# Performance work log

Measured on AMD Instinct MI355X. Metric: run time of the kernel, lower is better.

The kernel has to match this reference:

```python
import jax, jax.numpy as jnp
import numpy as np
import math

D_MODEL = 1024
N_HEADS = 16
D_K = D_MODEL // N_HEADS
LN_EPS = 1e-5


def _linear_params(key, d_in, d_out):
    # torch Linear stores weight as [out, in]; xavier_uniform init
    bound = math.sqrt(6.0 / (d_in + d_out))
    kw, kb = jax.random.split(key)
    W = jax.random.uniform(kw, (d_out, d_in), jnp.float32, -bound, bound)
    b = jnp.zeros((d_out,), jnp.float32)
    return W, b


def setup_inputs() -> dict:
    key = jax.random.key(0)
    ks = jax.random.split(key, 8)
    x = jax.random.normal(ks[0], (2, 2048, D_MODEL), jnp.float32)
    reasoning_state = jax.random.normal(ks[1], (2, D_MODEL), jnp.float32)
    Wq, bq = _linear_params(ks[2], D_MODEL, D_MODEL)
    Wk, bk = _linear_params(ks[3], D_MODEL, D_MODEL)
    Wv, bv = _linear_params(ks[4], D_MODEL, D_MODEL)
    Wr, br = _linear_params(ks[5], D_MODEL, D_MODEL)
    Wo, bo = _linear_params(ks[6], D_MODEL, D_MODEL)
    ln_g = jnp.ones((D_MODEL,), jnp.float32)
    ln_b = jnp.zeros((D_MODEL,), jnp.float32)
    return {"x": x, "reasoning_state": reasoning_state,
            "Wq": Wq, "bq": bq, "Wk": Wk, "bk": bk, "Wv": Wv, "bv": bv,
            "Wr": Wr, "br": br, "Wo": Wo, "bo": bo, "ln_g": ln_g, "ln_b": ln_b}


def reference(x, reasoning_state, Wq, bq, Wk, bk, Wv, bv, Wr, br, Wo, bo, ln_g, ln_b):
    B, S, D = x.shape
    H, dk = N_HEADS, D_K

    def proj(z, W, b):  # torch Linear: z @ W.T + b
        return z @ W.T + b

    # [B, H, S, dk]
    Q = proj(x, Wq, bq).reshape(B, S, H, dk).transpose(0, 2, 1, 3)
    K = proj(x, Wk, bk).reshape(B, S, H, dk).transpose(0, 2, 1, 3)
    V = proj(x, Wv, bv).reshape(B, S, H, dk).transpose(0, 2, 1, 3)

    scores = jnp.einsum('bhsd,bhtd->bhst', Q, K) / math.sqrt(dk)

    # reasoning bias: R is [B, H, 1, dk]; Q @ R^T -> [B, H, S, 1], broadcast over keys
    R = proj(reasoning_state, Wr, br).reshape(B, 1, H, dk).transpose(0, 2, 1, 3)
    scores = scores + jnp.einsum('bhsd,bhud->bhsu', Q, R)  # u == 1, broadcasts

    attn = jax.nn.softmax(scores, axis=-1)
    context = jnp.einsum('bhst,bhtd->bshd', attn, V).reshape(B, S, D)
    out = proj(context, Wo, bo)

    # residual + LayerNorm
    y = out + x
    mu = jnp.mean(y, axis=-1, keepdims=True)
    var = jnp.var(y, axis=-1, keepdims=True)
    y = (y - mu) * jax.lax.rsqrt(var + LN_EPS) * ln_g + ln_b
    return (y, attn)
```

## Files before the change

kernel.cpp:

```cpp
#include <hip/hip_runtime.h>
#include <hip/hip_bf16.h>

#define DM 1024
#define NH 16
#define DKK 64
#define SL 2048
#define NBATCH 2
#define NR (NBATCH*SL)

typedef __attribute__((ext_vector_type(8))) __bf16 bf16x8;
typedef __attribute__((ext_vector_type(4))) float f32x4;
using bf16 = __hip_bfloat16;

__global__ __launch_bounds__(256) void cvt_kernel(const float* __restrict__ src,
                                                  bf16* __restrict__ dst, int n4) {
  int stride = gridDim.x * blockDim.x;
  for (int i = blockIdx.x * blockDim.x + threadIdx.x; i < n4; i += stride) {
    float4 v = ((const float4*)src)[i];
    union { bf16 h[4]; ushort4 u; } un;
    un.h[0] = __float2bfloat16(v.x);
    un.h[1] = __float2bfloat16(v.y);
    un.h[2] = __float2bfloat16(v.z);
    un.h[3] = __float2bfloat16(v.w);
    ((ushort4*)dst)[i] = un.u;
  }
}

__global__ __launch_bounds__(256) void cvt4_kernel(
    const float* __restrict__ s0, const float* __restrict__ s1,
    const float* __restrict__ s2, const float* __restrict__ s3,
    bf16* __restrict__ d0, bf16* __restrict__ d1,
    bf16* __restrict__ d2, bf16* __restrict__ d3) {
  const int z = blockIdx.y;
  const float* src = (z == 0) ? s0 : (z == 1) ? s1 : (z == 2) ? s2 : s3;
  bf16* dst = (z == 0) ? d0 : (z == 1) ? d1 : (z == 2) ? d2 : d3;
  const int n4 = DM * DM / 4;
  int stride = gridDim.x * blockDim.x;
  for (int i = blockIdx.x * blockDim.x + threadIdx.x; i < n4; i += stride) {
    float4 v = ((const float4*)src)[i];
    union { bf16 h[4]; ushort4 u; } un;
    un.h[0] = __float2bfloat16(v.x);
    un.h[1] = __float2bfloat16(v.y);
    un.h[2] = __float2bfloat16(v.z);
    un.h[3] = __float2bfloat16(v.w);
    ((ushort4*)dst)[i] = un.u;
  }
}

__device__ __forceinline__ void gemm_core(const bf16* __restrict__ A, const bf16* __restrict__ W,
                                          int rowStart, int colStart,
                                          bf16* As, bf16* Bs, f32x4 acc[4][4]) {
  const int t = threadIdx.x;
  const int lane = t & 63, w = t >> 6;
  const int lg = lane & 15, lh = lane >> 4;
  const int wm = (w >> 1) * 64, wn = (w & 1) * 64;
#pragma unroll
  for (int i = 0; i < 4; ++i)
#pragma unroll
    for (int j = 0; j < 4; ++j) acc[i][j] = (f32x4){0.f, 0.f, 0.f, 0.f};

  for (int kt = 0; kt < DM / 32; ++kt) {
    int kb = kt * 32;
#pragma unroll
    for (int q = 0; q < 2; ++q) {
      int idx = q * 256 + t;
      int row = idx >> 2;
      int ce = (idx & 3) * 8;
      const bf16* ga = A + (size_t)(rowStart + row) * DM + kb + ce;
      const bf16* gb = W + (size_t)(colStart + row) * DM + kb + ce;
      int ldsbase = (q * 256 + w * 64) * 8;
      __builtin_amdgcn_global_load_lds((const __attribute__((address_space(1))) void*)ga,
                                       (__attribute__((address_space(3))) void*)(As + ldsbase),
                                       16, 0, 0);
      __builtin_amdgcn_global_load_lds((const __attribute__((address_space(1))) void*)gb,
                                       (__attribute__((address_space(3))) void*)(Bs + ldsbase),
                                       16, 0, 0);
    }
    __syncthreads();
    bf16x8 af[4], bfr[4];
#pragma unroll
    for (int i = 0; i < 4; ++i)
      af[i] = *(const bf16x8*)(As + (wm + i * 16 + lg) * 32 + 8 * lh);
#pragma unroll
    for (int j = 0; j < 4; ++j)
      bfr[j] = *(const bf16x8*)(Bs + (wn + j * 16 + lg) * 32 + 8 * lh);
#pragma unroll
    for (int i = 0; i < 4; ++i)
#pragma unroll
      for (int j = 0; j < 4; ++j)
        acc[i][j] = __builtin_amdgcn_mfma_f32_16x16x32_bf16(af[i], bfr[j], acc[i][j], 0, 0, 0);
    __syncthreads();
  }
}

__global__ __launch_bounds__(256) void gemm_qkv_kernel(
    const bf16* __restrict__ xb,
    const bf16* __restrict__ Wqb, const bf16* __restrict__ Wkb, const bf16* __restrict__ Wvb,
    const float* __restrict__ bq, const float* __restrict__ bk, const float* __restrict__ bv,
    bf16* __restrict__ Qb, bf16* __restrict__ Kb, bf16* __restrict__ Vt) {
  __shared__ bf16 As[128 * 32], Bs[128 * 32];
  const int z = blockIdx.z;
  const bf16* W = (z == 0) ? Wqb : (z == 1) ? Wkb : Wvb;
  const float* bias = (z == 0) ? bq : (z == 1) ? bk : bv;
  int rowStart = blockIdx.y * 128, colStart = blockIdx.x * 128;
  f32x4 acc[4][4];
  gemm_core(xb, W, rowStart, colStart, As, Bs, acc);

  const int t = threadIdx.x, lane = t & 63, w = t >> 6;
  const int lg = lane & 15, lh = lane >> 4;
  const int wm = (w >> 1) * 64, wn = (w & 1) * 64;
  if (z < 2) {
    bf16* out = (z == 0) ? Qb : Kb;
    const float sc = (z == 0) ? 0.125f : 1.0f;
#pragma unroll
    for (int i = 0; i < 4; ++i)
#pragma unroll
      for (int j = 0; j < 4; ++j) {
        int col = colStart + wn + j * 16 + lg;
        float bb = bias[col];
#pragma unroll
        for (int r = 0; r < 4; ++r) {
          int row = rowStart + wm + i * 16 + 4 * lh + r;
          out[(size_t)row * DM + col] = __float2bfloat16((acc[i][j][r] + bb) * sc);
        }
      }
  } else {
#pragma unroll
    for (int i = 0; i < 4; ++i)
#pragma unroll
      for (int j = 0; j < 4; ++j) {
        int col = colStart + wn + j * 16 + lg;
        int hh = col >> 6, d = col & 63;
        float bb = bias[col];
#pragma unroll
        for (int r = 0; r < 4; ++r) {
          int row = rowStart + wm + i * 16 + 4 * lh + r;
          int bb_i = row >> 11, s = row & 2047;
          Vt[(((size_t)(bb_i * NH + hh)) * DKK + d) * SL + s] = __float2bfloat16(acc[i][j][r] + bb);
        }
      }
  }
}

__global__ __launch_bounds__(256, 2) void attn_kernel(
    const bf16* __restrict__ Qb, const bf16* __restrict__ Kb, const bf16* __restrict__ Vt,
    float* __restrict__ attn_out, bf16* __restrict__ ctxb) {
  __shared__ bf16 Ps[128 * 128];
  __shared__ float sl[2 * 128];
  const int t = threadIdx.x, lane = t & 63, w = t >> 6;
  const int lg = lane & 15, lh = lane >> 4;

  const int L = blockIdx.x;
  const int xcd = L & 7, s_in = L >> 3;
  const int bh = xcd * 4 + (s_in >> 4);
  const int qtile = s_in & 15;
  const int b = bh >> 4, h = bh & 15;
  const int qbase = qtile * 128;
  const int wr = w >> 1, wc = w & 1;

  bf16x8 qf[4][2];
#pragma unroll
  for (int i = 0; i < 4; ++i)
#pragma unroll
    for (int ks = 0; ks < 2; ++ks)
      qf[i][ks] = *(const bf16x8*)(Qb +
          (size_t)(b * SL + qbase + wr * 64 + i * 16 + lg) * DM + h * DKK + ks * 32 + 8 * lh);

  const bf16* Kbase = Kb + (size_t)b * SL * DM + h * DKK;
  const bf16* Vtb = Vt + (size_t)bh * DKK * SL;

  float lsum[4] = {0.f, 0.f, 0.f, 0.f};
  for (int kt = 0; kt < 16; ++kt) {
    bf16x8 kf[4][2];
#pragma unroll
    for (int j = 0; j < 4; ++j)
#pragma unroll
      for (int ks = 0; ks < 2; ++ks)
        kf[j][ks] = *(const bf16x8*)(Kbase +
            (size_t)(kt * 128 + wc * 64 + j * 16 + lg) * DM + ks * 32 + 8 * lh);
    f32x4 s[4][4];
    __builtin_amdgcn_s_setprio(1);
#pragma unroll
    for (int i = 0; i < 4; ++i)
#pragma unroll
      for (int j = 0; j < 4; ++j) {
        f32x4 z = (f32x4){0.f, 0.f, 0.f, 0.f};
        z = __builtin_amdgcn_mfma_f32_16x16x32_bf16(kf[j][0], qf[i][0], z, 0, 0, 0);
        s[i][j] = __builtin_amdgcn_mfma_f32_16x16x32_bf16(kf[j][1], qf[i][1], z, 0, 0, 0);
      }
    __builtin_amdgcn_s_setprio(0);
#pragma unroll
    for (int i = 0; i < 4; ++i)
#pragma unroll
      for (int j = 0; j < 4; ++j)
#pragma unroll
        for (int r = 0; r < 4; ++r) lsum[i] += __expf(s[i][j][r]);
  }
#pragma unroll
  for (int i = 0; i < 4; ++i) {
    lsum[i] += __shfl_xor(lsum[i], 16);
    lsum[i] += __shfl_xor(lsum[i], 32);
  }
  if (lh == 0) {
#pragma unroll
    for (int i = 0; i < 4; ++i) sl[wc * 128 + wr * 64 + i * 16 + lg] = lsum[i];
  }
  __syncthreads();
  float linv[4];
#pragma unroll
  for (int i = 0; i < 4; ++i) {
    int q = wr * 64 + i * 16 + lg;
    linv[i] = 1.f / (sl[q] + sl[128 + q]);
  }
  __syncthreads();

  f32x4 cacc[4][2];
#pragma unroll
  for (int i = 0; i < 4; ++i) {
    cacc[i][0] = (f32x4){0.f, 0.f, 0.f, 0.f};
    cacc[i][1] = (f32x4){0.f, 0.f, 0.f, 0.f};
  }
  float* attn_base = attn_out + (size_t)bh * SL * SL;
  char* Pb = (char*)Ps;

  for (int kt = 0; kt < 16; ++kt) {
    bf16x8 kf[4][2];
#pragma unroll
    for (int j = 0; j < 4; ++j)
#pragma unroll
      for (int ks = 0; ks < 2; ++ks)
        kf[j][ks] = *(const bf16x8*)(Kbase +
            (size_t)(kt * 128 + wc * 64 + j * 16 + lg) * DM + ks * 32 + 8 * lh);
    f32x4 s[4][4];
    __builtin_amdgcn_s_setprio(1);
#pragma unroll
    for (int i = 0; i < 4; ++i)
#pragma unroll
      for (int j = 0; j < 4; ++j) {
        f32x4 z = (f32x4){0.f, 0.f, 0.f, 0.f};
        z = __builtin_amdgcn_mfma_f32_16x16x32_bf16(kf[j][0], qf[i][0], z, 0, 0, 0);
        s[i][j] = __builtin_amdgcn_mfma_f32_16x16x32_bf16(kf[j][1], qf[i][1], z, 0, 0, 0);
      }
    __builtin_amdgcn_s_setprio(0);
#pragma unroll
    for (int i = 0; i < 4; ++i) {
      const int q = wr * 64 + i * 16 + lg;
      const int swz = (q & 7) << 4;
#pragma unroll
      for (int j = 0; j < 4; ++j) {
        const int sk0 = wc * 64 + j * 16 + 4 * lh;
        f32x4 p4;
        p4[0] = __expf(s[i][j][0]) * linv[i];
        p4[1] = __expf(s[i][j][1]) * linv[i];
        p4[2] = __expf(s[i][j][2]) * linv[i];
        p4[3] = __expf(s[i][j][3]) * linv[i];
        __builtin_nontemporal_store(p4,
            (f32x4*)(attn_base + (size_t)(qbase + q) * SL + kt * 128 + sk0));
        union { bf16 h[4]; ushort4 u; } un;
        un.h[0] = __float2bfloat16(p4[0]);
        un.h[1] = __float2bfloat16(p4[1]);
        un.h[2] = __float2bfloat16(p4[2]);
        un.h[3] = __float2bfloat16(p4[3]);
        *(ushort4*)(Pb + ((q * 256 + sk0 * 2) ^ swz)) = un.u;
      }
    }
    __syncthreads();
    __builtin_amdgcn_s_setprio(1);
#pragma unroll
    for (int ks = 0; ks < 4; ++ks) {
      bf16x8 pf[4];
#pragma unroll
      for (int i = 0; i < 4; ++i) {
        const int q = wr * 64 + i * 16 + lg;
        pf[i] = *(const bf16x8*)(Pb + ((q * 256 + ks * 64 + lh * 16) ^ ((q & 7) << 4)));
      }
      bf16x8 vf[2];
#pragma unroll
      for (int jd = 0; jd < 2; ++jd)
        vf[jd] = *(const bf16x8*)(Vtb +
            (size_t)(wc * 32 + jd * 16 + lg) * SL + kt * 128 + ks * 32 + 8 * lh);
#pragma unroll
      for (int i = 0; i < 4; ++i)
#pragma unroll
        for (int jd = 0; jd < 2; ++jd)
          cacc[i][jd] = __builtin_amdgcn_mfma_f32_16x16x32_bf16(pf[i], vf[jd], cacc[i][jd], 0, 0, 0);
    }
    __builtin_amdgcn_s_setprio(0);
    __syncthreads();
  }

#pragma unroll
  for (int i = 0; i < 4; ++i)
#pragma unroll
    for (int jd = 0; jd < 2; ++jd)
#pragma unroll
      for (int r = 0; r < 4; ++r) {
        int row = qbase + wr * 64 + i * 16 + 4 * lh + r;
        int d = wc * 32 + jd * 16 + lg;
        ctxb[(size_t)(b * SL + row) * DM + h * DKK + d] = __float2bfloat16(cacc[i][jd][r]);
      }
}

__global__ __launch_bounds__(256) void gemm_o_kernel(
    const bf16* __restrict__ ctxb, const bf16* __restrict__ Wob, const float* __restrict__ bo,
    const float* __restrict__ xf, float* __restrict__ ypre) {
  __shared__ bf16 As[128 * 32], Bs[64 * 32];
  const int t = threadIdx.x, lane = t & 63, w = t >> 6;
  const int lg = lane & 15, lh = lane >> 4;
  const int wm = (w >> 1) * 64, wn = (w & 1) * 32;
  int rowStart = blockIdx.y * 128, colStart = blockIdx.x * 64;
  f32x4 acc[4][2];
#pragma unroll
  for (int i = 0; i < 4; ++i)
#pragma unroll
    for (int j = 0; j < 2; ++j) acc[i][j] = (f32x4){0.f, 0.f, 0.f, 0.f};

  for (int kt = 0; kt < DM / 32; ++kt) {
    int kb = kt * 32;
#pragma unroll
    for (int q = 0; q < 2; ++q) {
      int idx = q * 256 + t;
      int row = idx >> 2;
      int ce = (idx & 3) * 8;
      const bf16* ga = ctxb + (size_t)(rowStart + row) * DM + kb + ce;
      int ldsbase = (q * 256 + w * 64) * 8;
      __builtin_amdgcn_global_load_lds((const __attribute__((address_space(1))) void*)ga,
                                       (__attribute__((address_space(3))) void*)(As + ldsbase),
                                       16, 0, 0);
    }
    {
      int row = t >> 2, ce = (t & 3) * 8;
      const bf16* gb = Wob + (size_t)(colStart + row) * DM + kb + ce;
      int ldsbase = (w * 64) * 8;
      __builtin_amdgcn_global_load_lds((const __attribute__((address_space(1))) void*)gb,
                                       (__attribute__((address_space(3))) void*)(Bs + ldsbase),
                                       16, 0, 0);
    }
    __syncthreads();
    bf16x8 af[4], bfr[2];
#pragma unroll
    for (int i = 0; i < 4; ++i)
      af[i] = *(const bf16x8*)(As + (wm + i * 16 + lg) * 32 + 8 * lh);
#pragma unroll
    for (int j = 0; j < 2; ++j)
      bfr[j] = *(const bf16x8*)(Bs + (wn + j * 16 + lg) * 32 + 8 * lh);
#pragma unroll
    for (int i = 0; i < 4; ++i)
#pragma unroll
      for (int j = 0; j < 2; ++j)
        acc[i][j] = __builtin_amdgcn_mfma_f32_16x16x32_bf16(af[i], bfr[j], acc[i][j], 0, 0, 0);
    __syncthreads();
  }
#pragma unroll
  for (int i = 0; i < 4; ++i)
#pragma unroll
    for (int j = 0; j < 2; ++j) {
      int col = colStart + wn + j * 16 + lg;
      float bb = bo[col];
#pragma unroll
      for (int r = 0; r < 4; ++r) {
        int row = rowStart + wm + i * 16 + 4 * lh + r;
        ypre[(size_t)row * DM + col] = acc[i][j][r] + bb + xf[(size_t)row * DM + col];
      }
    }
}

__global__ __launch_bounds__(256) void ln_kernel(const float* __restrict__ ypre,
                                                 const float* __restrict__ g,
                                                 const float* __restrict__ bta,
                                                 float* __restrict__ out) {
  int row = blockIdx.x;
  const float* yr = ypre + (size_t)row * DM;
  int t = threadIdx.x;
  float4 v = *(const float4*)(yr + t * 4);
  float s = v.x + v.y + v.z + v.w;
  float ss = v.x * v.x + v.y * v.y + v.z * v.z + v.w * v.w;
#pragma unroll
  for (int off = 1; off < 64; off <<= 1) {
    s += __shfl_xor(s, off);
    ss += __shfl_xor(ss, off);
  }
  __shared__ float red[8];
  int w = t >> 6, lane = t & 63;
  if (lane == 0) { red[w] = s; red[4 + w] = ss; }
  __syncthreads();
  s = red[0] + red[1] + red[2] + red[3];
  ss = red[4] + red[5] + red[6] + red[7];
  float mu = s * (1.f / (float)DM);
  float var = ss * (1.f / (float)DM) - mu * mu;
  float rstd = rsqrtf(var + 1e-5f);
  float4 gv = *(const float4*)(g + t * 4);
  float4 bv = *(const float4*)(bta + t * 4);
  float4 o;
  o.x = (v.x - mu) * rstd * gv.x + bv.x;
  o.y = (v.y - mu) * rstd * gv.y + bv.y;
  o.z = (v.z - mu) * rstd * gv.z + bv.z;
  o.w = (v.w - mu) * rstd * gv.w + bv.w;
  *(float4*)(out + (size_t)row * DM + t * 4) = o;
}

extern "C" void kernel_launch(void* const* d_in, const int* in_sizes, int n_in,
                              void* d_out, int out_size, void* d_ws, size_t ws_size,
                              hipStream_t stream) {
  (void)in_sizes; (void)n_in; (void)out_size; (void)ws_size;
  const float* x = (const float*)d_in[0];
  const float* Wq = (const float*)d_in[2];
  const float* bq = (const float*)d_in[3];
  const float* Wk = (const float*)d_in[4];
  const float* bk = (const float*)d_in[5];
  const float* Wv = (const float*)d_in[6];
  const float* bv = (const float*)d_in[7];
  const float* Wo = (const float*)d_in[10];
  const float* bo = (const float*)d_in[11];
  const float* ln_g = (const float*)d_in[12];
  const float* ln_b = (const float*)d_in[13];
  float* out = (float*)d_out;

  char* ws = (char*)d_ws;
  const size_t MB = 1ull << 20;
  bf16* xb   = (bf16*)(ws + 0 * MB);
  bf16* Wqb  = (bf16*)(ws + 8 * MB);
  bf16* Wkb  = (bf16*)(ws + 10 * MB);
  bf16* Wvb  = (bf16*)(ws + 12 * MB);
  bf16* Wob  = (bf16*)(ws + 14 * MB);
  bf16* Qb   = (bf16*)(ws + 16 * MB);
  bf16* Kb   = (bf16*)(ws + 24 * MB);
  bf16* Vt   = (bf16*)(ws + 32 * MB);
  bf16* ctxb = (bf16*)(ws + 40 * MB);
  float* ypre = (float*)(ws + 48 * MB);

  float* y_out = out;
  float* attn_out = out + (size_t)NR * DM;

  cvt_kernel<<<2048, 256, 0, stream>>>(x, xb, NR * DM / 4);
  cvt4_kernel<<<dim3(256, 4), 256, 0, stream>>>(Wq, Wk, Wv, Wo, Wqb, Wkb, Wvb, Wob);

  gemm_qkv_kernel<<<dim3(8, 32, 3), 256, 0, stream>>>(xb, Wqb, Wkb, Wvb, bq, bk, bv, Qb, Kb, Vt);
  attn_kernel<<<512, 256, 0, stream>>>(Qb, Kb, Vt, attn_out, ctxb);
  gemm_o_kernel<<<dim3(16, 32), 256, 0, stream>>>(ctxb, Wob, bo, x, ypre);
  ln_kernel<<<4096, 256, 0, stream>>>(ypre, ln_g, ln_b, y_out);
}
```

Before: 308.2 us.

## Single-pass attention with full-row LDS probabilities and coalesced V transpose

Attention now computes QK once per 32-row query tile, storing unnormalized exp2 probabilities in bf16 in a 128KB LDS buffer, then normalizes and streams them to the fp32 output. The PV product is split across 8 waves by key range and reduced through LDS. V-transpose stores in the QKV GEMM are staged through swizzled LDS to give coalesced 16-byte writes, and the Q scale folds in log2(e). This removes the second QK recompute but lowers occupancy through the large LDS use, and it rounds the output probabilities through bf16.

```diff
diff --git a/kernel.cpp b/kernel.cpp
--- a/kernel.cpp
+++ b/kernel.cpp
@@ -11,6 +11,8 @@
 typedef __attribute__((ext_vector_type(8))) __bf16 bf16x8;
 typedef __attribute__((ext_vector_type(4))) float f32x4;
 using bf16 = __hip_bfloat16;
+
+#define QSCALE 0.18033688011112042f
 
 __global__ __launch_bounds__(256) void cvt_kernel(const float* __restrict__ src,
                                                   bf16* __restrict__ dst, int n4) {
@@ -98,7 +100,9 @@
     const bf16* __restrict__ Wqb, const bf16* __restrict__ Wkb, const bf16* __restrict__ Wvb,
     const float* __restrict__ bq, const float* __restrict__ bk, const float* __restrict__ bv,
     bf16* __restrict__ Qb, bf16* __restrict__ Kb, bf16* __restrict__ Vt) {
-  __shared__ bf16 As[128 * 32], Bs[128 * 32];
+  __shared__ bf16 smem[128 * 128];
+  bf16* As = smem;
+  bf16* Bs = smem + 4096;
   const int z = blockIdx.z;
   const bf16* W = (z == 0) ? Wqb : (z == 1) ? Wkb : Wvb;
   const float* bias = (z == 0) ? bq : (z == 1) ? bk : bv;
@@ -111,7 +115,7 @@
   const int wm = (w >> 1) * 64, wn = (w & 1) * 64;
   if (z < 2) {
     bf16* out = (z == 0) ? Qb : Kb;
-    const float sc = (z == 0) ? 0.125f : 1.0f;
+    const float sc = (z == 0) ? QSCALE : 1.0f;
 #pragma unroll
     for (int i = 0; i < 4; ++i)
 #pragma unroll
@@ -125,180 +129,196 @@
         }
       }
   } else {
+    char* T = (char*)smem;
 #pragma unroll
     for (int i = 0; i < 4; ++i)
 #pragma unroll
       for (int j = 0; j < 4; ++j) {
-        int col = colStart + wn + j * 16 + lg;
-        int hh = col >> 6, d = col & 63;
-        float bb = bias[col];
-#pragma unroll
-        for (int r = 0; r < 4; ++r) {
-          int row = rowStart + wm + i * 16 + 4 * lh + r;
-          int bb_i = row >> 11, s = row & 2047;
-          Vt[(((size_t)(bb_i * NH + hh)) * DKK + d) * SL + s] = __float2bfloat16(acc[i][j][r] + bb);
+        int col = wn + j * 16 + lg;
+        float bb = bias[colStart + col];
+        const int swz = (col & 7) << 4;
+#pragma unroll
+        for (int r2 = 0; r2 < 4; r2 += 2) {
+          int row = wm + i * 16 + 4 * lh + r2;
+          union { bf16 hh[2]; unsigned u; } un;
+          un.hh[0] = __float2bfloat16(acc[i][j][r2] + bb);
+          un.hh[1] = __float2bfloat16(acc[i][j][r2 + 1] + bb);
+          *(unsigned*)(T + ((col * 256 + row * 2) ^ swz)) = un.u;
         }
       }
-  }
-}
-
-__global__ __launch_bounds__(256, 2) void attn_kernel(
+    __syncthreads();
+    const int b_i = rowStart >> 11;
+    const int sbase = rowStart & 2047;
+#pragma unroll
+    for (int rd = 0; rd < 8; ++rd) {
+      int d_loc = rd * 16 + (t >> 4);
+      int s8 = (t & 15) * 8;
+      bf16x8 v = *(const bf16x8*)(T + ((d_loc * 256 + s8 * 2) ^ ((d_loc & 7) << 4)));
+      int col = colStart + d_loc;
+      int h2 = col >> 6, d = col & 63;
+      *(bf16x8*)(Vt + ((size_t)(b_i * NH + h2) * DKK + d) * SL + sbase + s8) = v;
+    }
+  }
+}
+
+__global__ __launch_bounds__(512, 2) void attn2_kernel(
     const bf16* __restrict__ Qb, const bf16* __restrict__ Kb, const bf16* __restrict__ Vt,
     float* __restrict__ attn_out, bf16* __restrict__ ctxb) {
-  __shared__ bf16 Ps[128 * 128];
-  __shared__ float sl[2 * 128];
+  __shared__ bf16 Ps[32 * 2048];
+  __shared__ float sl_s[8 * 32];
+  __shared__ float linv_s[32];
   const int t = threadIdx.x, lane = t & 63, w = t >> 6;
   const int lg = lane & 15, lh = lane >> 4;
 
   const int L = blockIdx.x;
-  const int xcd = L & 7, s_in = L >> 3;
-  const int bh = xcd * 4 + (s_in >> 4);
-  const int qtile = s_in & 15;
+  const int xcd = L & 7, idx = L >> 3;
+  const int bh = xcd * 4 + (idx >> 6);
+  const int qt = idx & 63;
   const int b = bh >> 4, h = bh & 15;
-  const int qbase = qtile * 128;
-  const int wr = w >> 1, wc = w & 1;
-
-  bf16x8 qf[4][2];
-#pragma unroll
-  for (int i = 0; i < 4; ++i)
+  const int qbase = qt * 32;
+
+  const bf16* Kbase = Kb + (size_t)b * SL * DM + h * DKK;
+  const bf16* Vtb = Vt + (size_t)bh * DKK * SL;
+  char* Pb = (char*)Ps;
+  const int kw = w * 256;
+
+  bf16x8 qf[2][2];
+#pragma unroll
+  for (int i = 0; i < 2; ++i)
 #pragma unroll
     for (int ks = 0; ks < 2; ++ks)
       qf[i][ks] = *(const bf16x8*)(Qb +
-          (size_t)(b * SL + qbase + wr * 64 + i * 16 + lg) * DM + h * DKK + ks * 32 + 8 * lh);
-
-  const bf16* Kbase = Kb + (size_t)b * SL * DM + h * DKK;
-  const bf16* Vtb = Vt + (size_t)bh * DKK * SL;
-
-  float lsum[4] = {0.f, 0.f, 0.f, 0.f};
-  for (int kt = 0; kt < 16; ++kt) {
-    bf16x8 kf[4][2];
-#pragma unroll
-    for (int j = 0; j < 4; ++j)
+          (size_t)(b * SL + qbase + i * 16 + lg) * DM + h * DKK + ks * 32 + 8 * lh);
+
+  float lsum[2] = {0.f, 0.f};
+  for (int kt = 0; kt < 8; ++kt) {
+    const int kb = kw + kt * 32;
+    bf16x8 kf[2][2];
+#pragma unroll
+    for (int jj = 0; jj < 2; ++jj)
 #pragma unroll
       for (int ks = 0; ks < 2; ++ks)
-        kf[j][ks] = *(const bf16x8*)(Kbase +
-            (size_t)(kt * 128 + wc * 64 + j * 16 + lg) * DM + ks * 32 + 8 * lh);
-    f32x4 s[4][4];
+        kf[jj][ks] = *(const bf16x8*)(Kbase +
+            (size_t)(kb + jj * 16 + lg) * DM + ks * 32 + 8 * lh);
+    f32x4 s[2][2];
     __builtin_amdgcn_s_setprio(1);
 #pragma unroll
-    for (int i = 0; i < 4; ++i)
-#pragma unroll
-      for (int j = 0; j < 4; ++j) {
+    for (int i = 0; i < 2; ++i)
+#pragma unroll
+      for (int jj = 0; jj < 2; ++jj) {
         f32x4 z = (f32x4){0.f, 0.f, 0.f, 0.f};
-        z = __builtin_amdgcn_mfma_f32_16x16x32_bf16(kf[j][0], qf[i][0], z, 0, 0, 0);
-        s[i][j] = __builtin_amdgcn_mfma_f32_16x16x32_bf16(kf[j][1], qf[i][1], z, 0, 0, 0);
+        z = __builtin_amdgcn_mfma_f32_16x16x32_bf16(kf[jj][0], qf[i][0], z, 0, 0, 0);
+        s[i][jj] = __builtin_amdgcn_mfma_f32_16x16x32_bf16(kf[jj][1], qf[i][1], z, 0, 0, 0);
       }
     __builtin_amdgcn_s_setprio(0);
 #pragma unroll
-    for (int i = 0; i < 4; ++i)
-#pragma unroll
-      for (int j = 0; j < 4; ++j)
-#pragma unroll
-        for (int r = 0; r < 4; ++r) lsum[i] += __expf(s[i][j][r]);
-  }
-#pragma unroll
-  for (int i = 0; i < 4; ++i) {
+    for (int i = 0; i < 2; ++i) {
+      const int q = i * 16 + lg;
+      const int swz = (q & 7) << 4;
+#pragma unroll
+      for (int jj = 0; jj < 2; ++jj) {
+        const int key0 = kb + jj * 16 + 4 * lh;
+        float p0 = exp2f(s[i][jj][0]);
+        float p1 = exp2f(s[i][jj][1]);
+        float p2 = exp2f(s[i][jj][2]);
+        float p3 = exp2f(s[i][jj][3]);
+        lsum[i] += (p0 + p1) + (p2 + p3);
+        union { bf16 hh[4]; ushort4 u4; } un;
+        un.hh[0] = __float2bfloat16(p0);
+        un.hh[1] = __float2bfloat16(p1);
+        un.hh[2] = __float2bfloat16(p2);
+        un.hh[3] = __float2bfloat16(p3);
+        *(ushort4*)(Pb + ((q * 4096 + key0 * 2) ^ swz)) = un.u4;
+      }
+    }
+  }
+#pragma unroll
+  for (int i = 0; i < 2; ++i) {
     lsum[i] += __shfl_xor(lsum[i], 16);
     lsum[i] += __shfl_xor(lsum[i], 32);
   }
   if (lh == 0) {
-#pragma unroll
-    for (int i = 0; i < 4; ++i) sl[wc * 128 + wr * 64 + i * 16 + lg] = lsum[i];
+    sl_s[w * 32 + lg] = lsum[0];
+    sl_s[w * 32 + 16 + lg] = lsum[1];
   }
   __syncthreads();
-  float linv[4];
-#pragma unroll
-  for (int i = 0; i < 4; ++i) {
-    int q = wr * 64 + i * 16 + lg;
-    linv[i] = 1.f / (sl[q] + sl[128 + q]);
+  if (t < 32) {
+    float tot = 0.f;
+#pragma unroll
+    for (int w8 = 0; w8 < 8; ++w8) tot += sl_s[w8 * 32 + t];
+    linv_s[t] = 1.f / tot;
   }
   __syncthreads();
 
-  f32x4 cacc[4][2];
-#pragma unroll
-  for (int i = 0; i < 4; ++i) {
-    cacc[i][0] = (f32x4){0.f, 0.f, 0.f, 0.f};
-    cacc[i][1] = (f32x4){0.f, 0.f, 0.f, 0.f};
-  }
-  float* attn_base = attn_out + (size_t)bh * SL * SL;
-  char* Pb = (char*)Ps;
-
-  for (int kt = 0; kt < 16; ++kt) {
-    bf16x8 kf[4][2];
-#pragma unroll
-    for (int j = 0; j < 4; ++j)
-#pragma unroll
-      for (int ks = 0; ks < 2; ++ks)
-        kf[j][ks] = *(const bf16x8*)(Kbase +
-            (size_t)(kt * 128 + wc * 64 + j * 16 + lg) * DM + ks * 32 + 8 * lh);
-    f32x4 s[4][4];
+  float* attn_base = attn_out + (size_t)bh * SL * SL + (size_t)qbase * SL;
+#pragma unroll
+  for (int rd = 0; rd < 16; ++rd) {
+    int id2 = rd * 512 + t;
+    int q = id2 >> 8;
+    int kcol = (id2 & 255) * 8;
+    union { bf16x8 v; ushort us[8]; } pu;
+    pu.v = *(const bf16x8*)(Pb + ((q * 4096 + kcol * 2) ^ ((q & 7) << 4)));
+    float li = linv_s[q];
+    f32x4 lo, hi;
+#pragma unroll
+    for (int e = 0; e < 4; ++e) {
+      lo[e] = __uint_as_float((unsigned)pu.us[e] << 16) * li;
+      hi[e] = __uint_as_float((unsigned)pu.us[e + 4] << 16) * li;
+    }
+    f32x4* dst = (f32x4*)(attn_base + (size_t)q * SL + kcol);
+    __builtin_nontemporal_store(lo, dst);
+    __builtin_nontemporal_store(hi, dst + 1);
+  }
+
+  f32x4 acc[2][4];
+#pragma unroll
+  for (int i = 0; i < 2; ++i)
+#pragma unroll
+    for (int jd = 0; jd < 4; ++jd) acc[i][jd] = (f32x4){0.f, 0.f, 0.f, 0.f};
+  for (int ks8 = 0; ks8 < 8; ++ks8) {
+    const int kb = kw + ks8 * 32;
+    bf16x8 pf[2];
+#pragma unroll
+    for (int i = 0; i < 2; ++i) {
+      const int q = i * 16 + lg;
+      pf[i] = *(const bf16x8*)(Pb + ((q * 4096 + (kb + 8 * lh) * 2) ^ ((q & 7) << 4)));
+    }
+    bf16x8 vf[4];
+#pragma unroll
+    for (int jd = 0; jd < 4; ++jd)
+      vf[jd] = *(const bf16x8*)(Vtb + (size_t)(jd * 16 + lg) * SL + kb + 8 * lh);
     __builtin_amdgcn_s_setprio(1);
 #pragma unroll
-    for (int i = 0; i < 4; ++i)
-#pragma unroll
-      for (int j = 0; j < 4; ++j) {
-        f32x4 z = (f32x4){0.f, 0.f, 0.f, 0.f};
-        z = __builtin_amdgcn_mfma_f32_16x16x32_bf16(kf[j][0], qf[i][0], z, 0, 0, 0);
-        s[i][j] = __builtin_amdgcn_mfma_f32_16x16x32_bf16(kf[j][1], qf[i][1], z, 0, 0, 0);
-      }
+    for (int i = 0; i < 2; ++i)
+#pragma unroll
+      for (int jd = 0; jd < 4; ++jd)
+        acc[i][jd] = __builtin_amdgcn_mfma_f32_16x16x32_bf16(pf[i], vf[jd], acc[i][jd], 0, 0, 0);
     __builtin_amdgcn_s_setprio(0);
-#pragma unroll
-    for (int i = 0; i < 4; ++i) {
-      const int q = wr * 64 + i * 16 + lg;
-      const int swz = (q & 7) << 4;
-#pragma unroll
-      for (int j = 0; j < 4; ++j) {
-        const int sk0 = wc * 64 + j * 16 + 4 * lh;
-        f32x4 p4;
-        p4[0] = __expf(s[i][j][0]) * linv[i];
-        p4[1] = __expf(s[i][j][1]) * linv[i];
-        p4[2] = __expf(s[i][j][2]) * linv[i];
-        p4[3] = __expf(s[i][j][3]) * linv[i];
-        __builtin_nontemporal_store(p4,
-            (f32x4*)(attn_base + (size_t)(qbase + q) * SL + kt * 128 + sk0));
-        union { bf16 h[4]; ushort4 u; } un;
-        un.h[0] = __float2bfloat16(p4[0]);
-        un.h[1] = __float2bfloat16(p4[1]);
-        un.h[2] = __float2bfloat16(p4[2]);
-        un.h[3] = __float2bfloat16(p4[3]);
-        *(ushort4*)(Pb + ((q * 256 + sk0 * 2) ^ swz)) = un.u;
-      }
-    }
-    __syncthreads();
-    __builtin_amdgcn_s_setprio(1);
-#pragma unroll
-    for (int ks = 0; ks < 4; ++ks) {
-      bf16x8 pf[4];
-#pragma unroll
-      for (int i = 0; i < 4; ++i) {
-        const int q = wr * 64 + i * 16 + lg;
-        pf[i] = *(const bf16x8*)(Pb + ((q * 256 + ks * 64 + lh * 16) ^ ((q & 7) << 4)));
-      }
-      bf16x8 vf[2];
-#pragma unroll
-      for (int jd = 0; jd < 2; ++jd)
-        vf[jd] = *(const bf16x8*)(Vtb +
-            (size_t)(wc * 32 + jd * 16 + lg) * SL + kt * 128 + ks * 32 + 8 * lh);
-#pragma unroll
-      for (int i = 0; i < 4; ++i)
-#pragma unroll
-        for (int jd = 0; jd < 2; ++jd)
-          cacc[i][jd] = __builtin_amdgcn_mfma_f32_16x16x32_bf16(pf[i], vf[jd], cacc[i][jd], 0, 0, 0);
-    }
-    __builtin_amdgcn_s_setprio(0);
-    __syncthreads();
-  }
-
-#pragma unroll
-  for (int i = 0; i < 4; ++i)
-#pragma unroll
-    for (int jd = 0; jd < 2; ++jd)
-#pragma unroll
-      for (int r = 0; r < 4; ++r) {
-        int row = qbase + wr * 64 + i * 16 + 4 * lh + r;
-        int d = wc * 32 + jd * 16 + lg;
-        ctxb[(size_t)(b * SL + row) * DM + h * DKK + d] = __float2bfloat16(cacc[i][jd][r]);
-      }
+  }
+  __syncthreads();
+
+  float* part = (float*)Ps;
+#pragma unroll
+  for (int i = 0; i < 2; ++i)
+#pragma unroll
+    for (int jd = 0; jd < 4; ++jd)
+#pragma unroll
+      for (int r = 0; r < 4; ++r)
+        part[w * 2048 + (i * 16 + 4 * lh + r) * 64 + jd * 16 + lg] = acc[i][jd][r];
+  __syncthreads();
+
+  {
+    int e = t * 4;
+    int q = e >> 6, d0 = e & 63;
+    f32x4 sum = (f32x4){0.f, 0.f, 0.f, 0.f};
+#pragma unroll
+    for (int w8 = 0; w8 < 8; ++w8) sum += *(const f32x4*)(part + w8 * 2048 + e);
+    float li = linv_s[q];
+    union { bf16 hh[4]; ushort4 u4; } un;
+#pragma unroll
+    for (int r = 0; r < 4; ++r) un.hh[r] = __float2bfloat16(sum[r] * li);
+    *(ushort4*)(ctxb + (size_t)(b * SL + qbase + q) * DM + h * DKK + d0) = un.u4;
+  }
 }
 
 __global__ __launch_bounds__(256) void gemm_o_kernel(
@@ -436,7 +456,7 @@
   cvt4_kernel<<<dim3(256, 4), 256, 0, stream>>>(Wq, Wk, Wv, Wo, Wqb, Wkb, Wvb, Wob);
 
   gemm_qkv_kernel<<<dim3(8, 32, 3), 256, 0, stream>>>(xb, Wqb, Wkb, Wvb, bq, bk, bv, Qb, Kb, Vt);
-  attn_kernel<<<512, 256, 0, stream>>>(Qb, Kb, Vt, attn_out, ctxb);
+  attn2_kernel<<<2048, 512, 0, stream>>>(Qb, Kb, Vt, attn_out, ctxb);
   gemm_o_kernel<<<dim3(16, 32), 256, 0, stream>>>(ctxb, Wob, bo, x, ypre);
   ln_kernel<<<4096, 256, 0, stream>>>(ypre, ln_g, ln_b, y_out);
 }
```

Result: slower. 316.7 us (+2.8%).

## Split attention into denominator and write kernels, stage V transpose through LDS

Applied to the files above, without the earlier changes.

Splits the two-pass attention into one kernel that computes softmax denominators and one that writes probabilities and context. The split frees the write kernel's registers and LDS from the reduction state. The V-transpose epilogue now stages through swizzled shared memory so global stores are coalesced 16-byte writes along the sequence. Q is pre-scaled by log2(e)/8 so exp2f can replace __expf, and the per-tile barriers become explicit lgkmcnt waits plus s_barrier, dropping the trailing sync. Risks include an extra launch, an extra global round trip for the denominators, and a possible race on the P buffer now that the end-of-loop barrier is gone.

```diff
diff --git a/kernel.cpp b/kernel.cpp
--- a/kernel.cpp
+++ b/kernel.cpp
@@ -11,6 +11,14 @@
 typedef __attribute__((ext_vector_type(8))) __bf16 bf16x8;
 typedef __attribute__((ext_vector_type(4))) float f32x4;
 using bf16 = __hip_bfloat16;
+
+#define QSCALE 0.18033688011112042f
+
+#define LGKM_BARRIER() do { \
+  asm volatile("s_waitcnt lgkmcnt(0)" ::: "memory"); \
+  __builtin_amdgcn_s_barrier(); \
+  __builtin_amdgcn_sched_barrier(0); \
+} while (0)
 
 __global__ __launch_bounds__(256) void cvt_kernel(const float* __restrict__ src,
                                                   bf16* __restrict__ dst, int n4) {
@@ -98,7 +106,9 @@
     const bf16* __restrict__ Wqb, const bf16* __restrict__ Wkb, const bf16* __restrict__ Wvb,
     const float* __restrict__ bq, const float* __restrict__ bk, const float* __restrict__ bv,
     bf16* __restrict__ Qb, bf16* __restrict__ Kb, bf16* __restrict__ Vt) {
-  __shared__ bf16 As[128 * 32], Bs[128 * 32];
+  __shared__ bf16 smem[128 * 128];
+  bf16* As = smem;
+  bf16* Bs = smem + 4096;
   const int z = blockIdx.z;
   const bf16* W = (z == 0) ? Wqb : (z == 1) ? Wkb : Wvb;
   const float* bias = (z == 0) ? bq : (z == 1) ? bk : bv;
@@ -111,7 +121,7 @@
   const int wm = (w >> 1) * 64, wn = (w & 1) * 64;
   if (z < 2) {
     bf16* out = (z == 0) ? Qb : Kb;
-    const float sc = (z == 0) ? 0.125f : 1.0f;
+    const float sc = (z == 0) ? QSCALE : 1.0f;
 #pragma unroll
     for (int i = 0; i < 4; ++i)
 #pragma unroll
@@ -125,31 +135,45 @@
         }
       }
   } else {
+    char* T = (char*)smem;
+    __syncthreads();
 #pragma unroll
     for (int i = 0; i < 4; ++i)
 #pragma unroll
       for (int j = 0; j < 4; ++j) {
-        int col = colStart + wn + j * 16 + lg;
-        int hh = col >> 6, d = col & 63;
-        float bb = bias[col];
-#pragma unroll
-        for (int r = 0; r < 4; ++r) {
-          int row = rowStart + wm + i * 16 + 4 * lh + r;
-          int bb_i = row >> 11, s = row & 2047;
-          Vt[(((size_t)(bb_i * NH + hh)) * DKK + d) * SL + s] = __float2bfloat16(acc[i][j][r] + bb);
+        int col = wn + j * 16 + lg;
+        float bb = bias[colStart + col];
+        const int swz = (col & 7) << 4;
+#pragma unroll
+        for (int r2 = 0; r2 < 4; r2 += 2) {
+          int row = wm + i * 16 + 4 * lh + r2;
+          union { bf16 hh[2]; unsigned u; } un;
+          un.hh[0] = __float2bfloat16(acc[i][j][r2] + bb);
+          un.hh[1] = __float2bfloat16(acc[i][j][r2 + 1] + bb);
+          *(unsigned*)(T + ((col * 256 + row * 2) ^ swz)) = un.u;
         }
       }
-  }
-}
-
-__global__ __launch_bounds__(256, 2) void attn_kernel(
-    const bf16* __restrict__ Qb, const bf16* __restrict__ Kb, const bf16* __restrict__ Vt,
-    float* __restrict__ attn_out, bf16* __restrict__ ctxb) {
-  __shared__ bf16 Ps[128 * 128];
+    __syncthreads();
+    const int b_i = rowStart >> 11;
+    const int sbase = rowStart & 2047;
+#pragma unroll
+    for (int rd = 0; rd < 8; ++rd) {
+      int d_loc = rd * 16 + (t >> 4);
+      int s8 = (t & 15) * 8;
+      bf16x8 v = *(const bf16x8*)(T + ((d_loc * 256 + s8 * 2) ^ ((d_loc & 7) << 4)));
+      int col = colStart + d_loc;
+      int h2 = col >> 6, d = col & 63;
+      *(bf16x8*)(Vt + ((size_t)(b_i * NH + h2) * DKK + d) * SL + sbase + s8) = v;
+    }
+  }
+}
+
+__global__ __launch_bounds__(256, 2) void attn_den_kernel(
+    const bf16* __restrict__ Qb, const bf16* __restrict__ Kb,
+    float* __restrict__ linv_g) {
   __shared__ float sl[2 * 128];
   const int t = threadIdx.x, lane = t & 63, w = t >> 6;
   const int lg = lane & 15, lh = lane >> 4;
-
   const int L = blockIdx.x;
   const int xcd = L & 7, s_in = L >> 3;
   const int bh = xcd * 4 + (s_in >> 4);
@@ -167,7 +191,6 @@
           (size_t)(b * SL + qbase + wr * 64 + i * 16 + lg) * DM + h * DKK + ks * 32 + 8 * lh);
 
   const bf16* Kbase = Kb + (size_t)b * SL * DM + h * DKK;
-  const bf16* Vtb = Vt + (size_t)bh * DKK * SL;
 
   float lsum[4] = {0.f, 0.f, 0.f, 0.f};
   for (int kt = 0; kt < 16; ++kt) {
@@ -194,7 +217,7 @@
 #pragma unroll
       for (int j = 0; j < 4; ++j)
 #pragma unroll
-        for (int r = 0; r < 4; ++r) lsum[i] += __expf(s[i][j][r]);
+        for (int r = 0; r < 4; ++r) lsum[i] += exp2f(s[i][j][r]);
   }
 #pragma unroll
   for (int i = 0; i < 4; ++i) {
@@ -206,13 +229,43 @@
     for (int i = 0; i < 4; ++i) sl[wc * 128 + wr * 64 + i * 16 + lg] = lsum[i];
   }
   __syncthreads();
+  if (t < 128) {
+    linv_g[(size_t)bh * SL + qbase + t] = 1.f / (sl[t] + sl[128 + t]);
+  }
+}
+
+__global__ __launch_bounds__(256, 2) void attn_wr_kernel(
+    const bf16* __restrict__ Qb, const bf16* __restrict__ Kb, const bf16* __restrict__ Vt,
+    const float* __restrict__ linv_g,
+    float* __restrict__ attn_out, bf16* __restrict__ ctxb) {
+  __shared__ bf16 Ps[128 * 128];
+  const int t = threadIdx.x, lane = t & 63, w = t >> 6;
+  const int lg = lane & 15, lh = lane >> 4;
+  const int L = blockIdx.x;
+  const int xcd = L & 7, s_in = L >> 3;
+  const int bh = xcd * 4 + (s_in >> 4);
+  const int qtile = s_in & 15;
+  const int b = bh >> 4, h = bh & 15;
+  const int qbase = qtile * 128;
+  const int wr = w >> 1, wc = w & 1;
+
+  bf16x8 qf[4][2];
+#pragma unroll
+  for (int i = 0; i < 4; ++i)
+#pragma unroll
+    for (int ks = 0; ks < 2; ++ks)
+      qf[i][ks] = *(const bf16x8*)(Qb +
+          (size_t)(b * SL + qbase + wr * 64 + i * 16 + lg) * DM + h * DKK + ks * 32 + 8 * lh);
+
   float linv[4];
 #pragma unroll
-  for (int i = 0; i < 4; ++i) {
-    int q = wr * 64 + i * 16 + lg;
-    linv[i] = 1.f / (sl[q] + sl[128 + q]);
-  }
-  __syncthreads();
+  for (int i = 0; i < 4; ++i)
+    linv[i] = linv_g[(size_t)bh * SL + qbase + wr * 64 + i * 16 + lg];
+
+  const bf16* Kbase = Kb + (size_t)b * SL * DM + h * DKK;
+  const bf16* Vtb = Vt + (size_t)bh * DKK * SL;
+  float* attn_base = attn_out + (size_t)bh * SL * SL;
+  char* Pb = (char*)Ps;
 
   f32x4 cacc[4][2];
 #pragma unroll
@@ -220,8 +273,6 @@
     cacc[i][0] = (f32x4){0.f, 0.f, 0.f, 0.f};
     cacc[i][1] = (f32x4){0.f, 0.f, 0.f, 0.f};
   }
-  float* attn_base = attn_out + (size_t)bh * SL * SL;
-  char* Pb = (char*)Ps;
 
   for (int kt = 0; kt < 16; ++kt) {
     bf16x8 kf[4][2];
@@ -242,6 +293,9 @@
         s[i][j] = __builtin_amdgcn_mfma_f32_16x16x32_bf16(kf[j][1], qf[i][1], z, 0, 0, 0);
       }
     __builtin_amdgcn_s_setprio(0);
+
+    LGKM_BARRIER();
+
 #pragma unroll
     for (int i = 0; i < 4; ++i) {
       const int q = wr * 64 + i * 16 + lg;
@@ -250,21 +304,23 @@
       for (int j = 0; j < 4; ++j) {
         const int sk0 = wc * 64 + j * 16 + 4 * lh;
         f32x4 p4;
-        p4[0] = __expf(s[i][j][0]) * linv[i];
-        p4[1] = __expf(s[i][j][1]) * linv[i];
-        p4[2] = __expf(s[i][j][2]) * linv[i];
-        p4[3] = __expf(s[i][j][3]) * linv[i];
+        p4[0] = exp2f(s[i][j][0]) * linv[i];
+        p4[1] = exp2f(s[i][j][1]) * linv[i];
+        p4[2] = exp2f(s[i][j][2]) * linv[i];
+        p4[3] = exp2f(s[i][j][3]) * linv[i];
         __builtin_nontemporal_store(p4,
             (f32x4*)(attn_base + (size_t)(qbase + q) * SL + kt * 128 + sk0));
-        union { bf16 h[4]; ushort4 u; } un;
-        un.h[0] = __float2bfloat16(p4[0]);
-        un.h[1] = __float2bfloat16(p4[1]);
-        un.h[2] = __float2bfloat16(p4[2]);
-        un.h[3] = __float2bfloat16(p4[3]);
-        *(ushort4*)(Pb + ((q * 256 + sk0 * 2) ^ swz)) = un.u;
-      }
-    }
-    __syncthreads();
+        union { bf16 hh[4]; ushort4 u4; } un;
+        un.hh[0] = __float2bfloat16(p4[0]);
+        un.hh[1] = __float2bfloat16(p4[1]);
+        un.hh[2] = __float2bfloat16(p4[2]);
+        un.hh[3] = __float2bfloat16(p4[3]);
+        *(ushort4*)(Pb + ((q * 256 + sk0 * 2) ^ swz)) = un.u4;
+      }
+    }
+
+    LGKM_BARRIER();
+
     __builtin_amdgcn_s_setprio(1);
 #pragma unroll
     for (int ks = 0; ks < 4; ++ks) {
@@ -286,7 +342,6 @@
           cacc[i][jd] = __builtin_amdgcn_mfma_f32_16x16x32_bf16(pf[i], vf[jd], cacc[i][jd], 0, 0, 0);
     }
     __builtin_amdgcn_s_setprio(0);
-    __syncthreads();
   }
 
 #pragma unroll
@@ -428,6 +483,7 @@
   bf16* Vt   = (bf16*)(ws + 32 * MB);
   bf16* ctxb = (bf16*)(ws + 40 * MB);
   float* ypre = (float*)(ws + 48 * MB);
+  float* linv_g = (float*)(ws + 64 * MB);
 
   float* y_out = out;
   float* attn_out = out + (size_t)NR * DM;
@@ -436,7 +492,8 @@
   cvt4_kernel<<<dim3(256, 4), 256, 0, stream>>>(Wq, Wk, Wv, Wo, Wqb, Wkb, Wvb, Wob);
 
   gemm_qkv_kernel<<<dim3(8, 32, 3), 256, 0, stream>>>(xb, Wqb, Wkb, Wvb, bq, bk, bv, Qb, Kb, Vt);
-  attn_kernel<<<512, 256, 0, stream>>>(Qb, Kb, Vt, attn_out, ctxb);
+  attn_den_kernel<<<512, 256, 0, stream>>>(Qb, Kb, linv_g);
+  attn_wr_kernel<<<512, 256, 0, stream>>>(Qb, Kb, Vt, linv_g, attn_out, ctxb);
   gemm_o_kernel<<<dim3(16, 32), 256, 0, stream>>>(ctxb, Wob, bo, x, ypre);
   ln_kernel<<<4096, 256, 0, stream>>>(ypre, ln_g, ln_b, y_out);
 }
```

New measurement: 304.9 us. No clear change (-1.1%).
